# Kernel optimization log

Measured on AMD Instinct MI355X. Metric: run time of the kernel, lower is better.

Reference implementation:

```python
import jax, jax.numpy as jnp
import numpy as np

T = 512        # sentence length
V = 50000      # word vocab
NT = 50        # tag vocab
WD = 200       # word_dims
TD = 50        # tag_dims
U = 512        # lstm_units (per direction)
HID = 1024     # hidden_units
SOUT = 2       # struct_out
LOUT = 56      # label_out
NS = 8192      # number of struct span-sets
NL = 8192      # number of label span-sets
KS = 4         # struct_spans
KL = 3         # label_spans


def _spans(kl, kr, n, k):
    lefts = jax.random.randint(kl, (n, k), 1, T - 2)
    rights = jnp.minimum(lefts + jax.random.randint(kr, (n, k), 0, 16), T - 2)
    return lefts.astype(jnp.int32), rights.astype(jnp.int32)


def setup_inputs() -> dict:
    key = jax.random.key(0)
    ks = jax.random.split(key, 40)
    s = 0.02
    inp = {
        'word_inds': jax.random.randint(ks[0], (T,), 0, V).astype(jnp.int32),
        'tag_inds': jax.random.randint(ks[1], (T,), 0, NT).astype(jnp.int32),
        'struct_targets': jax.random.randint(ks[2], (NS,), 0, SOUT).astype(jnp.int32),
        'label_targets': jax.random.randint(ks[3], (NL,), 0, LOUT).astype(jnp.int32),
    }
    inp['struct_lefts'], inp['struct_rights'] = _spans(ks[4], ks[5], NS, KS)
    inp['label_lefts'], inp['label_rights'] = _spans(ks[6], ks[7], NL, KL)
    inp['W_word'] = jax.random.normal(ks[8], (V, WD), jnp.float32) * s
    inp['W_tag'] = jax.random.normal(ks[9], (NT, TD), jnp.float32) * s
    # LSTM params, PyTorch layout: W_ih [4U, in], W_hh [4U, U], bias [4U] (b_ih+b_hh fused)
    d0, d1 = WD + TD, 2 * U
    i = 10
    for name, din in [('l0f', d0), ('l0b', d0), ('l1f', d1), ('l1b', d1)]:
        inp['Wih_' + name] = jax.random.normal(ks[i], (4 * U, din), jnp.float32) * s; i += 1
        inp['Whh_' + name] = jax.random.normal(ks[i], (4 * U, U), jnp.float32) * s; i += 1
        inp['b_' + name] = jnp.zeros((4 * U,), jnp.float32)
    inp['Ws1'] = jax.random.normal(ks[i], (HID, 2 * KS * U), jnp.float32) * s; i += 1
    inp['bs1'] = jnp.zeros((HID,), jnp.float32)
    inp['Ws2'] = jax.random.normal(ks[i], (SOUT, HID), jnp.float32) * s; i += 1
    inp['bs2'] = jnp.zeros((SOUT,), jnp.float32)
    inp['Wl1'] = jax.random.normal(ks[i], (HID, 2 * KL * U), jnp.float32) * s; i += 1
    inp['bl1'] = jnp.zeros((HID,), jnp.float32)
    inp['Wl2'] = jax.random.normal(ks[i], (LOUT, HID), jnp.float32) * s; i += 1
    inp['bl2'] = jnp.zeros((LOUT,), jnp.float32)
    return inp


def _lstm_dir(x, Wih, Whh, b, reverse):
    # x: [T, Din] -> h sequence [T, U]; gate order i,f,g,o (PyTorch)
    xg = x @ Wih.T + b  # [T, 4U]
    u = Whh.shape[1]
    def step(carry, xt):
        h, c = carry
        g = xt + h @ Whh.T
        gi, gf, gg, go = jnp.split(g, 4)
        i = jax.nn.sigmoid(gi); f = jax.nn.sigmoid(gf)
        gg = jnp.tanh(gg); o = jax.nn.sigmoid(go)
        c = f * c + i * gg
        h = o * jnp.tanh(c)
        return (h, c), h
    init = (jnp.zeros((u,), x.dtype), jnp.zeros((u,), x.dtype))
    _, hs = jax.lax.scan(step, init, xg, reverse=reverse)
    return hs


def _span_loss(fwd, back, lefts, rights, targets, W1, b1, W2, b2):
    n = lefts.shape[0]
    f = fwd[rights] - fwd[lefts - 1]          # [N, K, U]
    bk = back[lefts] - back[rights + 1]       # [N, K, U]
    h = jnp.concatenate([f.reshape(n, -1), bk.reshape(n, -1)], axis=1)
    h = jax.nn.relu(h @ W1.T + b1)
    scores = h @ W2.T + b2
    logp = jax.nn.log_softmax(scores, axis=-1)
    return -jnp.take_along_axis(logp, targets[:, None], axis=1)[:, 0]


def reference(word_inds, tag_inds, struct_lefts, struct_rights, struct_targets,
              label_lefts, label_rights, label_targets,
              W_word, W_tag,
              Wih_l0f, Whh_l0f, b_l0f, Wih_l0b, Whh_l0b, b_l0b,
              Wih_l1f, Whh_l1f, b_l1f, Wih_l1b, Whh_l1b, b_l1b,
              Ws1, bs1, Ws2, bs2, Wl1, bl1, Wl2, bl2):
    x = jnp.concatenate([W_word[word_inds], W_tag[tag_inds]], axis=1)  # [T, WD+TD]
    h0 = jnp.concatenate([_lstm_dir(x, Wih_l0f, Whh_l0f, b_l0f, False),
                          _lstm_dir(x, Wih_l0b, Whh_l0b, b_l0b, True)], axis=1)
    out = jnp.concatenate([_lstm_dir(h0, Wih_l1f, Whh_l1f, b_l1f, False),
                           _lstm_dir(h0, Wih_l1b, Whh_l1b, b_l1b, True)], axis=1)  # [T, 2U]
    fwd, back = out[:, :U], out[:, U:]
    sl = _span_loss(fwd, back, struct_lefts, struct_rights, struct_targets, Ws1, bs1, Ws2, bs2)
    ll = _span_loss(fwd, back, label_lefts, label_rights, label_targets, Wl1, bl1, Wl2, bl2)
    return jnp.concatenate([sl, ll]).mean()
```

## Files before the change

kernel.cpp:

```cpp
#include <hip/hip_runtime.h>

using u16 = unsigned short;
using u32 = unsigned int;
using u64 = unsigned long long;
typedef __attribute__((ext_vector_type(8))) short bf16x8;
typedef __attribute__((ext_vector_type(4))) float f32x4;

__device__ __forceinline__ u16 f2b(float f) {
  u32 u = __float_as_uint(f);
  return (u16)((u + 0x7fffu + ((u >> 16) & 1u)) >> 16);
}

static constexpr size_t HEX_SZ    = (size_t)513 * 512 * 4;
static constexpr size_t OFF_HEXF0 = 0;
static constexpr size_t OFF_HEXB0 = OFF_HEXF0 + HEX_SZ;
static constexpr size_t OFF_HEXF1 = OFF_HEXB0 + HEX_SZ;
static constexpr size_t OFF_HEXB1 = OFF_HEXF1 + HEX_SZ;
static constexpr size_t OFF_LACC  = OFF_HEXB1 + HEX_SZ;
static constexpr size_t OFF_CLAIM = OFF_LACC + 1024;
static constexpr size_t OFF_PROG  = OFF_CLAIM + 256;
static constexpr size_t ZERO_BYTES= OFF_PROG + 4 * 262144;
static constexpr size_t OFF_XB    = ZERO_BYTES;
static constexpr size_t OFF_WIH0F = OFF_XB    + (size_t)512*256*2;
static constexpr size_t OFF_WIH0B = OFF_WIH0F + (size_t)2048*256*2;
static constexpr size_t OFF_WIH1F = OFF_WIH0B + (size_t)2048*256*2;
static constexpr size_t OFF_WIH1B = OFF_WIH1F + (size_t)2048*1024*2;
static constexpr size_t OFF_BSALL = OFF_WIH1B + (size_t)2048*1024*2;
static constexpr size_t OFF_BLALL = OFF_BSALL + (size_t)8192*512*2;
static constexpr size_t OFF_HCAT0 = OFF_BLALL + (size_t)6144*512*2;
static constexpr size_t OFF_HCAT1 = OFF_HCAT0 + (size_t)512*1024*2;
static constexpr size_t OFF_XG0F  = OFF_HCAT1 + (size_t)512*1024*2;
static constexpr size_t OFF_XG0B  = OFF_XG0F  + (size_t)512*2048*4;
static constexpr size_t OFF_XG1F  = OFF_XG0B  + (size_t)512*2048*4;
static constexpr size_t OFF_XG1B  = OFF_XG1F  + (size_t)512*2048*4;
static constexpr size_t OFF_PFS   = OFF_XG1B  + (size_t)512*2048*4;
static constexpr size_t OFF_PBS   = OFF_PFS   + (size_t)512*4096*4;
static constexpr size_t OFF_PFL   = OFF_PBS   + (size_t)512*4096*4;
static constexpr size_t OFF_PBL   = OFF_PFL   + (size_t)512*3072*4;

__global__ __launch_bounds__(64) void k_embed(const int* __restrict__ wi, const int* __restrict__ ti,
                                              const float* __restrict__ Ww, const float* __restrict__ Wt,
                                              u16* __restrict__ x) {
  int t = blockIdx.x;
  int w = wi[t], tg = ti[t];
  for (int c = threadIdx.x; c < 256; c += 64) {
    float v = 0.f;
    if (c < 200) v = Ww[(size_t)w * 200 + c];
    else if (c < 250) v = Wt[(size_t)tg * 50 + (c - 200)];
    x[(size_t)t * 256 + c] = f2b(v);
  }
}

__global__ __launch_bounds__(256) void k_prep_all(const float* __restrict__ Wih_l0f, const float* __restrict__ Wih_l0b,
                                                  u16* __restrict__ wih0f, u16* __restrict__ wih0b,
                                                  const float* __restrict__ Wih_l1f, const float* __restrict__ Wih_l1b,
                                                  u16* __restrict__ wih1f, u16* __restrict__ wih1b,
                                                  const float* __restrict__ Ws1, u16* __restrict__ bsall,
                                                  const float* __restrict__ Wl1, u16* __restrict__ blall) {
  int i0 = blockIdx.x * 256 + threadIdx.x, stride = gridDim.x * 256;
  for (int i = i0; i < 2048 * 256; i += stride) {
    int n = i >> 8, k = i & 255;
    wih0f[i] = (k < 250) ? f2b(Wih_l0f[(size_t)n * 250 + k]) : (u16)0;
    wih0b[i] = (k < 250) ? f2b(Wih_l0b[(size_t)n * 250 + k]) : (u16)0;
  }
  for (int i = i0; i < 2048 * 1024; i += stride) {
    wih1f[i] = f2b(Wih_l1f[i]);
    wih1b[i] = f2b(Wih_l1b[i]);
  }
  for (int i = i0; i < 8 * 1024 * 512; i += stride) {
    int u = i & 511, nidx = i >> 9, k = nidx >> 10, h = nidx & 1023;
    bsall[i] = f2b(Ws1[(size_t)h * 4096 + k * 512 + u]);
  }
  for (int i = i0; i < 6 * 1024 * 512; i += stride) {
    int u = i & 511, nidx = i >> 9, k = nidx >> 10, h = nidx & 1023;
    blall[i] = f2b(Wl1[(size_t)h * 3072 + k * 512 + u]);
  }
}

#define AST 40
__device__ __forceinline__ void gemm_body(const u16* __restrict__ A, int lda,
                                          const u16* __restrict__ B, int ldb,
                                          float* __restrict__ C, int ldc,
                                          const float* __restrict__ bias, int K,
                                          int m0, int n0) {
  __shared__ u16 As[128 * AST];
  __shared__ u16 Bs[128 * AST];
  int tid = threadIdx.x;
  int lane = tid & 63, wave = tid >> 6;
  int wm = wave >> 1, wn = wave & 1;
  f32x4 z = {0.f, 0.f, 0.f, 0.f};
  f32x4 acc[4][4];
#pragma unroll
  for (int i = 0; i < 4; ++i)
#pragma unroll
    for (int j = 0; j < 4; ++j) acc[i][j] = z;

  for (int k0 = 0; k0 < K; k0 += 32) {
#pragma unroll
    for (int it = 0; it < 2; ++it) {
      int c = tid + it * 256;
      int row = c >> 2, cc = (c & 3) << 3;
      *(bf16x8*)&As[row * AST + cc] = *(const bf16x8*)&A[(size_t)(m0 + row) * lda + k0 + cc];
      *(bf16x8*)&Bs[row * AST + cc] = *(const bf16x8*)&B[(size_t)(n0 + row) * ldb + k0 + cc];
    }
    __syncthreads();
    int rA = lane & 15, kk = (lane >> 4) << 3;
    bf16x8 af[4], bg[4];
#pragma unroll
    for (int i = 0; i < 4; ++i) {
      af[i] = *(const bf16x8*)&As[(wm * 64 + i * 16 + rA) * AST + kk];
      bg[i] = *(const bf16x8*)&Bs[(wn * 64 + i * 16 + rA) * AST + kk];
    }
#pragma unroll
    for (int i = 0; i < 4; ++i)
#pragma unroll
      for (int j = 0; j < 4; ++j)
        acc[i][j] = __builtin_amdgcn_mfma_f32_16x16x32_bf16(af[i], bg[j], acc[i][j], 0, 0, 0);
    __syncthreads();
  }
  int rg = (lane >> 4) << 2;
#pragma unroll
  for (int i = 0; i < 4; ++i)
#pragma unroll
    for (int j = 0; j < 4; ++j) {
      int n = n0 + wn * 64 + j * 16 + (lane & 15);
      float bv = bias ? bias[n] : 0.f;
#pragma unroll
      for (int r = 0; r < 4; ++r) {
        int m = m0 + wm * 64 + i * 16 + rg + r;
        C[(size_t)m * ldc + n] = acc[i][j][r] + bv;
      }
    }
}

__global__ __launch_bounds__(256) void k_gemm2(const u16* A, int lda,
                                               const u16* B0, const u16* B1, int ldb,
                                               float* C0, float* C1, int ldc,
                                               const float* bias0, const float* bias1, int K) {
  int z = blockIdx.z;
  gemm_body(A, lda, z ? B1 : B0, ldb, z ? C1 : C0, ldc, z ? bias1 : bias0, K,
            blockIdx.y * 128, blockIdx.x * 128);
}

__global__ __launch_bounds__(256) void k_proj(const u16* hcat1, const u16* bsall, const u16* blall,
                                              float* Pfs, float* Pbs, float* Pfl, float* Pbl) {
  int z = blockIdx.z;
  if (z >= 2 && blockIdx.x >= 24) return;
  const u16* A = (z & 1) ? (hcat1 + 512) : hcat1;
  const u16* B; float* C; int N;
  if (z == 0)      { B = bsall;                        C = Pfs; N = 4096; }
  else if (z == 1) { B = bsall + (size_t)4096 * 512;   C = Pbs; N = 4096; }
  else if (z == 2) { B = blall;                        C = Pfl; N = 3072; }
  else             { B = blall + (size_t)3072 * 512;   C = Pbl; N = 3072; }
  gemm_body(A, 1024, B, 512, C, N, nullptr, 512, blockIdx.y * 128, blockIdx.x * 128);
}

template <bool FAST>
__device__ __forceinline__ void lstm_core(int dir, int slice,
                                          const float* __restrict__ xg, const float* __restrict__ whh,
                                          u32* __restrict__ hex, u32* __restrict__ prog,
                                          u16* __restrict__ hcat) {
  __shared__ __align__(16) u16 hw[4][2][512];
  int tid = threadIdx.x;
  int wave = tid >> 6, lane = tid & 63;
  int col = lane & 15, kgrp = lane >> 4;
  int u0 = slice * 32;
  int uw = u0 + 8 * wave;

  bf16x8 bfr[2][16];
#pragma unroll
  for (int ntl = 0; ntl < 2; ++ntl) {
    int gate = 2 * ntl + (col >> 3);
    int row = gate * 512 + uw + (col & 7);
    const float* wr = whh + (size_t)row * 512;
#pragma unroll
    for (int kt = 0; kt < 16; ++kt) {
      int k0 = kt * 32 + kgrp * 8;
      f32x4 w0 = *(const f32x4*)&wr[k0];
      f32x4 w1 = *(const f32x4*)&wr[k0 + 4];
      bf16x8 v;
      v[0] = (short)f2b(w0.x); v[1] = (short)f2b(w0.y);
      v[2] = (short)f2b(w0.z); v[3] = (short)f2b(w0.w);
      v[4] = (short)f2b(w1.x); v[5] = (short)f2b(w1.y);
      v[6] = (short)f2b(w1.z); v[7] = (short)f2b(w1.w);
      bfr[ntl][kt] = v;
    }
  }

  const u64 TAGM = 0x0000FFFF0000FFFFull;
  float creg = 0.f;
  u32 it = (u32)(slice * 4 + wave);
  for (int s = 0; s < 512; ++s) {
    int t = dir ? (511 - s) : s;
    int rrow = dir ? (t + 1) : t;
    int par = s & 1;

    const float* xr = &xg[(size_t)t * 2048 + uw + (lane & 7)];
    float xga = xr[0], xgb2 = xr[512], xgc = xr[1024], xgd = xr[1536];

    u64 w0, w1, w2, w3;
    if constexpr (FAST) {
      for (;;) {
        u32 idx = (it++) & 63u;
        u32 p;
        if (idx == 0u)
          p = __hip_atomic_load(&prog[lane & 15], __ATOMIC_RELAXED, __HIP_MEMORY_SCOPE_AGENT);
        else
          p = __hip_atomic_load(&prog[(size_t)idx * 1024 + (lane & 15)], __ATOMIC_RELAXED, __HIP_MEMORY_SCOPE_WORKGROUP);
        if (__all((int)(p >= (u32)s))) break;
      }
      asm volatile("" ::: "memory");
      const u64* hp = (const u64*)(hex + (size_t)rrow * 512) + lane * 4;
      w0 = __hip_atomic_load(hp + 0, __ATOMIC_RELAXED, __HIP_MEMORY_SCOPE_WORKGROUP);
      w1 = __hip_atomic_load(hp + 1, __ATOMIC_RELAXED, __HIP_MEMORY_SCOPE_WORKGROUP);
      w2 = __hip_atomic_load(hp + 2, __ATOMIC_RELAXED, __HIP_MEMORY_SCOPE_WORKGROUP);
      w3 = __hip_atomic_load(hp + 3, __ATOMIC_RELAXED, __HIP_MEMORY_SCOPE_WORKGROUP);
    } else {
      const u64* hp = (const u64*)(hex + (size_t)rrow * 512) + lane * 4;
      u64 expct = (u64)(u32)s | ((u64)(u32)s << 32);
      do {
        w0 = __hip_atomic_load(hp + 0, __ATOMIC_RELAXED, __HIP_MEMORY_SCOPE_AGENT);
        w1 = __hip_atomic_load(hp + 1, __ATOMIC_RELAXED, __HIP_MEMORY_SCOPE_AGENT);
        w2 = __hip_atomic_load(hp + 2, __ATOMIC_RELAXED, __HIP_MEMORY_SCOPE_AGENT);
        w3 = __hip_atomic_load(hp + 3, __ATOMIC_RELAXED, __HIP_MEMORY_SCOPE_AGENT);
      } while (((w0 & TAGM) != expct) | ((w1 & TAGM) != expct) |
               ((w2 & TAGM) != expct) | ((w3 & TAGM) != expct));
    }

    bf16x8 hv;
    hv[0] = (short)(u16)(w0 >> 16); hv[1] = (short)(u16)(w0 >> 48);
    hv[2] = (short)(u16)(w1 >> 16); hv[3] = (short)(u16)(w1 >> 48);
    hv[4] = (short)(u16)(w2 >> 16); hv[5] = (short)(u16)(w2 >> 48);
    hv[6] = (short)(u16)(w3 >> 16); hv[7] = (short)(u16)(w3 >> 48);
    *(bf16x8*)&hw[wave][par][lane * 8] = hv;

    const u16* hb = &hw[wave][par][0];
    f32x4 z4 = {0.f, 0.f, 0.f, 0.f};
    f32x4 acc0[4], acc1[4];
#pragma unroll
    for (int q = 0; q < 4; ++q) { acc0[q] = z4; acc1[q] = z4; }
#pragma unroll
    for (int kt = 0; kt < 16; ++kt) {
      bf16x8 a = *(const bf16x8*)&hb[kt * 32 + kgrp * 8];
      acc0[kt & 3] = __builtin_amdgcn_mfma_f32_16x16x32_bf16(a, bfr[0][kt], acc0[kt & 3], 0, 0, 0);
      acc1[kt & 3] = __builtin_amdgcn_mfma_f32_16x16x32_bf16(a, bfr[1][kt], acc1[kt & 3], 0, 0, 0);
    }
    float v0 = acc0[0].x + acc0[1].x + acc0[2].x + acc0[3].x;
    float v1 = acc1[0].x + acc1[1].x + acc1[2].x + acc1[3].x;
    float gfv = __shfl_xor(v0, 8);
    float gov = __shfl_xor(v1, 8);
    if (lane < 8) {
      float gi = v0 + xga, gf = gfv + xgb2, gg = v1 + xgc, go = gov + xgd;
      float iv = __builtin_amdgcn_rcpf(1.f + __expf(-gi));
      float fv = __builtin_amdgcn_rcpf(1.f + __expf(-gf));
      float gv = 1.f - 2.f * __builtin_amdgcn_rcpf(__expf(2.f * gg) + 1.f);
      float ov = __builtin_amdgcn_rcpf(1.f + __expf(-go));
      creg = fv * creg + iv * gv;
      float h = ov * (1.f - 2.f * __builtin_amdgcn_rcpf(__expf(2.f * creg) + 1.f));
      u16 hb16 = f2b(h);
      int wrow = dir ? t : (t + 1);
      u32 word = ((u32)hb16 << 16) | (u32)(s + 1);
      if constexpr (FAST)
        __hip_atomic_store(&hex[(size_t)wrow * 512 + uw + lane], word, __ATOMIC_RELAXED, __HIP_MEMORY_SCOPE_WORKGROUP);
      else
        __hip_atomic_store(&hex[(size_t)wrow * 512 + uw + lane], word, __ATOMIC_RELAXED, __HIP_MEMORY_SCOPE_AGENT);
      hcat[(size_t)t * 1024 + dir * 512 + uw + lane] = hb16;
    }
    if constexpr (FAST) {
      __syncthreads();
      if (wave == 0) {
        if (lane == 0)
          __hip_atomic_store(&prog[slice], (u32)(s + 1), __ATOMIC_RELAXED, __HIP_MEMORY_SCOPE_AGENT);
        else
          __hip_atomic_store(&prog[(size_t)lane * 1024 + slice], (u32)(s + 1), __ATOMIC_RELAXED, __HIP_MEMORY_SCOPE_WORKGROUP);
      }
    }
  }
}

__global__ __launch_bounds__(256, 1) void k_lstm(const float* __restrict__ xg_f, const float* __restrict__ xg_b,
                                                 const float* __restrict__ whh_f, const float* __restrict__ whh_b,
                                                 u32* __restrict__ hex_f, u32* __restrict__ hex_b,
                                                 u32* __restrict__ claim,
                                                 u32* __restrict__ prog_f, u32* __restrict__ prog_b,
                                                 u16* __restrict__ hcat) {
  __shared__ int sh[3];
  if (threadIdx.x == 0) {
    u32 xcd;
    asm volatile("s_getreg_b32 %0, hwreg(HW_REG_XCC_ID)" : "=s"(xcd));
    xcd &= 7u;
    u32 slot = __hip_atomic_fetch_add(&claim[xcd], 1u, __ATOMIC_RELAXED, __HIP_MEMORY_SCOPE_AGENT);
    u32 tot  = __hip_atomic_fetch_add(&claim[8], 1u, __ATOMIC_ACQ_REL, __HIP_MEMORY_SCOPE_AGENT);
    if (tot == (u32)gridDim.x - 1u) {
      u32 c0 = __hip_atomic_load(&claim[0], __ATOMIC_RELAXED, __HIP_MEMORY_SCOPE_AGENT);
      u32 c1 = __hip_atomic_load(&claim[1], __ATOMIC_RELAXED, __HIP_MEMORY_SCOPE_AGENT);
      __hip_atomic_store(&claim[9], (c0 >= 16u && c1 >= 16u) ? 1u : 2u,
                         __ATOMIC_RELEASE, __HIP_MEMORY_SCOPE_AGENT);
    }
    u32 m;
    do { m = __hip_atomic_load(&claim[9], __ATOMIC_ACQUIRE, __HIP_MEMORY_SCOPE_AGENT); } while (m == 0u);
    int dir = -1, slice = 0;
    if (m == 1u) {
      if (xcd == 0u && slot < 16u)      { dir = 0; slice = (int)slot; }
      else if (xcd == 1u && slot < 16u) { dir = 1; slice = (int)slot; }
    } else {
      u32 s2 = __hip_atomic_fetch_add(&claim[10], 1u, __ATOMIC_RELAXED, __HIP_MEMORY_SCOPE_AGENT);
      if (s2 < 32u) { dir = (int)(s2 >> 4); slice = (int)(s2 & 15u); }
    }
    sh[0] = dir; sh[1] = slice; sh[2] = (m == 1u) ? 1 : 0;
  }
  __syncthreads();
  int dir = sh[0], slice = sh[1], fast = sh[2];
  if (dir < 0) return;
  const float* xg  = dir ? xg_b : xg_f;
  const float* whh = dir ? whh_b : whh_f;
  u32* hex  = dir ? hex_b : hex_f;
  u32* prog = dir ? prog_b : prog_f;
  if (fast) lstm_core<true>(dir, slice, xg, whh, hex, prog, hcat);
  else      lstm_core<false>(dir, slice, xg, whh, hex, prog, hcat);
}

template <int KSP, int C>
__device__ __forceinline__ void span_body(int blk,
                                          const float* __restrict__ Pf, const float* __restrict__ Pb,
                                          const int* __restrict__ lefts, const int* __restrict__ rights,
                                          const int* __restrict__ tgts, const float* __restrict__ b1,
                                          const float* __restrict__ W2, const float* __restrict__ b2,
                                          float* __restrict__ loss_acc) {
  constexpr int NP = KSP * 1024;
  __shared__ float hid[4][1024];
  __shared__ float sc[4][64];
  int tid = threadIdx.x;
  int n0 = blk * 4;
  int d = tid * 4;
  f32x4 bv = *(const f32x4*)&b1[d];
#pragma unroll
  for (int ss = 0; ss < 4; ++ss) {
    int n = n0 + ss;
    f32x4 acc = bv;
#pragma unroll
    for (int k = 0; k < KSP; ++k) {
      int l = lefts[n * KSP + k], r = rights[n * KSP + k];
      f32x4 a1 = *(const f32x4*)&Pf[(size_t)r * NP + k * 1024 + d];
      f32x4 a2 = *(const f32x4*)&Pf[(size_t)(l - 1) * NP + k * 1024 + d];
      f32x4 a3 = *(const f32x4*)&Pb[(size_t)l * NP + k * 1024 + d];
      f32x4 a4 = *(const f32x4*)&Pb[(size_t)(r + 1) * NP + k * 1024 + d];
      acc += a1 - a2 + a3 - a4;
    }
    acc.x = fmaxf(acc.x, 0.f); acc.y = fmaxf(acc.y, 0.f);
    acc.z = fmaxf(acc.z, 0.f); acc.w = fmaxf(acc.w, 0.f);
    *(f32x4*)&hid[ss][d] = acc;
  }
  __syncthreads();
  int wave = tid >> 6, lane = tid & 63;
  for (int c = wave; c < C; c += 4) {
    float p0 = 0.f, p1 = 0.f, p2 = 0.f, p3 = 0.f;
    for (int i = lane; i < 1024; i += 64) {
      float w = W2[(size_t)c * 1024 + i];
      p0 += hid[0][i] * w; p1 += hid[1][i] * w; p2 += hid[2][i] * w; p3 += hid[3][i] * w;
    }
#pragma unroll
    for (int o = 32; o; o >>= 1) {
      p0 += __shfl_xor(p0, o); p1 += __shfl_xor(p1, o);
      p2 += __shfl_xor(p2, o); p3 += __shfl_xor(p3, o);
    }
    if (lane == 0) {
      sc[0][c] = p0 + b2[c]; sc[1][c] = p1 + b2[c];
      sc[2][c] = p2 + b2[c]; sc[3][c] = p3 + b2[c];
    }
  }
  __syncthreads();
  {
    int s = wave;
    float v = (lane < C) ? sc[s][lane] : -1e30f;
    float m = v;
#pragma unroll
    for (int o = 32; o; o >>= 1) m = fmaxf(m, __shfl_xor(m, o));
    float e = (lane < C) ? __expf(v - m) : 0.f;
#pragma unroll
    for (int o = 32; o; o >>= 1) e += __shfl_xor(e, o);
    if (lane == 0) {
      int tg = tgts[n0 + s];
      float loss = m + __logf(e) - sc[s][tg];
      atomicAdd(&loss_acc[(n0 + s) & 255], loss);
    }
  }
}

__global__ __launch_bounds__(256) void k_span_fused(const float* Pfs, const float* Pbs,
                                                    const int* s_l, const int* s_r, const int* s_tgt,
                                                    const float* bs1, const float* Ws2, const float* bs2,
                                                    const float* Pfl, const float* Pbl,
                                                    const int* l_l, const int* l_r, const int* l_tgt,
                                                    const float* bl1, const float* Wl2, const float* bl2,
                                                    float* lacc) {
  if (blockIdx.x < 2048)
    span_body<4, 2>(blockIdx.x, Pfs, Pbs, s_l, s_r, s_tgt, bs1, Ws2, bs2, lacc);
  else
    span_body<3, 56>(blockIdx.x - 2048, Pfl, Pbl, l_l, l_r, l_tgt, bl1, Wl2, bl2, lacc);
}

__global__ __launch_bounds__(256) void k_finalize(const float* __restrict__ acc, float* __restrict__ out) {
  int tid = threadIdx.x;
  __shared__ float s[4];
  float v = acc[tid];
#pragma unroll
  for (int o = 32; o; o >>= 1) v += __shfl_xor(v, o);
  if ((tid & 63) == 0) s[tid >> 6] = v;
  __syncthreads();
  if (tid == 0) out[0] = (s[0] + s[1] + s[2] + s[3]) * (1.0f / 16384.0f);
}

extern "C" void kernel_launch(void* const* d_in, const int* in_sizes, int n_in,
                              void* d_out, int out_size, void* d_ws, size_t ws_size,
                              hipStream_t stream) {
  (void)in_sizes; (void)n_in; (void)out_size; (void)ws_size;
  const int* word_inds = (const int*)d_in[0];
  const int* tag_inds  = (const int*)d_in[1];
  const int* s_tgt = (const int*)d_in[2];
  const int* l_tgt = (const int*)d_in[3];
  const int* s_l = (const int*)d_in[4];
  const int* s_r = (const int*)d_in[5];
  const int* l_l = (const int*)d_in[6];
  const int* l_r = (const int*)d_in[7];
  const float* W_word  = (const float*)d_in[8];
  const float* W_tag   = (const float*)d_in[9];
  const float* Wih_l0f = (const float*)d_in[10];
  const float* Whh_l0f = (const float*)d_in[11];
  const float* b_l0f   = (const float*)d_in[12];
  const float* Wih_l0b = (const float*)d_in[13];
  const float* Whh_l0b = (const float*)d_in[14];
  const float* b_l0b   = (const float*)d_in[15];
  const float* Wih_l1f = (const float*)d_in[16];
  const float* Whh_l1f = (const float*)d_in[17];
  const float* b_l1f   = (const float*)d_in[18];
  const float* Wih_l1b = (const float*)d_in[19];
  const float* Whh_l1b = (const float*)d_in[20];
  const float* b_l1b   = (const float*)d_in[21];
  const float* Ws1 = (const float*)d_in[22];
  const float* bs1 = (const float*)d_in[23];
  const float* Ws2 = (const float*)d_in[24];
  const float* bs2 = (const float*)d_in[25];
  const float* Wl1 = (const float*)d_in[26];
  const float* bl1 = (const float*)d_in[27];
  const float* Wl2 = (const float*)d_in[28];
  const float* bl2 = (const float*)d_in[29];

  char* ws = (char*)d_ws;
  u32* hexf0 = (u32*)(ws + OFF_HEXF0);
  u32* hexb0 = (u32*)(ws + OFF_HEXB0);
  u32* hexf1 = (u32*)(ws + OFF_HEXF1);
  u32* hexb1 = (u32*)(ws + OFF_HEXB1);
  float* lacc = (float*)(ws + OFF_LACC);
  u32* claim0 = (u32*)(ws + OFF_CLAIM);
  u32* claim1 = (u32*)(ws + OFF_CLAIM + 64);
  u32* progf0 = (u32*)(ws + OFF_PROG);
  u32* progb0 = (u32*)(ws + OFF_PROG + 262144);
  u32* progf1 = (u32*)(ws + OFF_PROG + 2 * 262144);
  u32* progb1 = (u32*)(ws + OFF_PROG + 3 * 262144);
  u16* xb    = (u16*)(ws + OFF_XB);
  u16* wih0f = (u16*)(ws + OFF_WIH0F);
  u16* wih0b = (u16*)(ws + OFF_WIH0B);
  u16* wih1f = (u16*)(ws + OFF_WIH1F);
  u16* wih1b = (u16*)(ws + OFF_WIH1B);
  u16* bsall = (u16*)(ws + OFF_BSALL);
  u16* blall = (u16*)(ws + OFF_BLALL);
  u16* hcat0 = (u16*)(ws + OFF_HCAT0);
  u16* hcat1 = (u16*)(ws + OFF_HCAT1);
  float* xg0f = (float*)(ws + OFF_XG0F);
  float* xg0b = (float*)(ws + OFF_XG0B);
  float* xg1f = (float*)(ws + OFF_XG1F);
  float* xg1b = (float*)(ws + OFF_XG1B);
  float* Pfs = (float*)(ws + OFF_PFS);
  float* Pbs = (float*)(ws + OFF_PBS);
  float* Pfl = (float*)(ws + OFF_PFL);
  float* Pbl = (float*)(ws + OFF_PBL);

  hipMemsetAsync(ws, 0, ZERO_BYTES, stream);

  k_embed<<<512, 64, 0, stream>>>(word_inds, tag_inds, W_word, W_tag, xb);
  k_prep_all<<<1024, 256, 0, stream>>>(Wih_l0f, Wih_l0b, wih0f, wih0b,
                                       Wih_l1f, Wih_l1b, wih1f, wih1b,
                                       Ws1, bsall, Wl1, blall);

  k_gemm2<<<dim3(16, 4, 2), 256, 0, stream>>>(xb, 256, wih0f, wih0b, 256, xg0f, xg0b, 2048, b_l0f, b_l0b, 256);
  k_lstm<<<256, 256, 0, stream>>>(xg0f, xg0b, Whh_l0f, Whh_l0b, hexf0, hexb0, claim0, progf0, progb0, hcat0);
  k_gemm2<<<dim3(16, 4, 2), 256, 0, stream>>>(hcat0, 1024, wih1f, wih1b, 1024, xg1f, xg1b, 2048, b_l1f, b_l1b, 1024);
  k_lstm<<<256, 256, 0, stream>>>(xg1f, xg1b, Whh_l1f, Whh_l1b, hexf1, hexb1, claim1, progf1, progb1, hcat1);

  k_proj<<<dim3(32, 4, 4), 256, 0, stream>>>(hcat1, bsall, blall, Pfs, Pbs, Pfl, Pbl);

  k_span_fused<<<4096, 256, 0, stream>>>(Pfs, Pbs, s_l, s_r, s_tgt, bs1, Ws2, bs2,
                                         Pfl, Pbl, l_l, l_r, l_tgt, bl1, Wl2, bl2, lacc);
  k_finalize<<<1, 256, 0, stream>>>(lacc, (float*)d_out);
}
```

Before: 2.008 ms.

## Replace LSTM progress-flag sync with tagged polling, bf16 projections, xg prefetch

The LSTM recurrence drops the per-step __syncthreads plus progress-counter broadcast. Each wave now polls the tagged h-exchange rows directly with sc0 loads, and every eighth retry falls back to an agent-scope shadow copy. Gate input terms are prefetched into LDS every 64 steps, the span projections are stored as bf16 to halve span-kernel traffic, and the large memset becomes a tiny zeroing kernel that clears only the boundary rows. The intent is to shorten the per-step serial latency of the recurrence, at the cost of extra duplicate stores, some visibility risk from the cache-level polling, and bf16 rounding on the projection outputs.

```diff
diff --git a/kernel.cpp b/kernel.cpp
--- a/kernel.cpp
+++ b/kernel.cpp
@@ -10,17 +10,20 @@
   u32 u = __float_as_uint(f);
   return (u16)((u + 0x7fffu + ((u >> 16) & 1u)) >> 16);
 }
+__device__ __forceinline__ float b2f(u16 v) { return __uint_as_float(((u32)v) << 16); }
 
 static constexpr size_t HEX_SZ    = (size_t)513 * 512 * 4;
 static constexpr size_t OFF_HEXF0 = 0;
 static constexpr size_t OFF_HEXB0 = OFF_HEXF0 + HEX_SZ;
 static constexpr size_t OFF_HEXF1 = OFF_HEXB0 + HEX_SZ;
 static constexpr size_t OFF_HEXB1 = OFF_HEXF1 + HEX_SZ;
-static constexpr size_t OFF_LACC  = OFF_HEXB1 + HEX_SZ;
+static constexpr size_t OFF_HSF0  = OFF_HEXB1 + HEX_SZ;
+static constexpr size_t OFF_HSB0  = OFF_HSF0  + HEX_SZ;
+static constexpr size_t OFF_HSF1  = OFF_HSB0  + HEX_SZ;
+static constexpr size_t OFF_HSB1  = OFF_HSF1  + HEX_SZ;
+static constexpr size_t OFF_LACC  = OFF_HSB1  + HEX_SZ;
 static constexpr size_t OFF_CLAIM = OFF_LACC + 1024;
-static constexpr size_t OFF_PROG  = OFF_CLAIM + 256;
-static constexpr size_t ZERO_BYTES= OFF_PROG + 4 * 262144;
-static constexpr size_t OFF_XB    = ZERO_BYTES;
+static constexpr size_t OFF_XB    = OFF_CLAIM + 256;
 static constexpr size_t OFF_WIH0F = OFF_XB    + (size_t)512*256*2;
 static constexpr size_t OFF_WIH0B = OFF_WIH0F + (size_t)2048*256*2;
 static constexpr size_t OFF_WIH1F = OFF_WIH0B + (size_t)2048*256*2;
@@ -34,9 +37,22 @@
 static constexpr size_t OFF_XG1F  = OFF_XG0B  + (size_t)512*2048*4;
 static constexpr size_t OFF_XG1B  = OFF_XG1F  + (size_t)512*2048*4;
 static constexpr size_t OFF_PFS   = OFF_XG1B  + (size_t)512*2048*4;
-static constexpr size_t OFF_PBS   = OFF_PFS   + (size_t)512*4096*4;
-static constexpr size_t OFF_PFL   = OFF_PBS   + (size_t)512*4096*4;
-static constexpr size_t OFF_PBL   = OFF_PFL   + (size_t)512*3072*4;
+static constexpr size_t OFF_PBS   = OFF_PFS   + (size_t)512*4096*2;
+static constexpr size_t OFF_PFL   = OFF_PBS   + (size_t)512*4096*2;
+static constexpr size_t OFF_PBL   = OFF_PFL   + (size_t)512*3072*2;
+
+__global__ __launch_bounds__(256) void k_zero(u32* hf0, u32* hb0, u32* hf1, u32* hb1,
+                                              u32* sf0, u32* sb0, u32* sf1, u32* sb1,
+                                              u32* lacc, u32* claims) {
+  int tid = threadIdx.x;
+  for (int i = tid; i < 512; i += 256) {
+    size_t o = (size_t)512 * 512 + i;
+    hf0[i] = 0; hf1[i] = 0; sf0[i] = 0; sf1[i] = 0;
+    hb0[o] = 0; hb1[o] = 0; sb0[o] = 0; sb1[o] = 0;
+  }
+  lacc[tid] = 0;
+  if (tid < 64) claims[tid] = 0;
+}
 
 __global__ __launch_bounds__(64) void k_embed(const int* __restrict__ wi, const int* __restrict__ ti,
                                               const float* __restrict__ Ww, const float* __restrict__ Wt,
@@ -78,9 +94,10 @@
 }
 
 #define AST 40
+template <bool BF16OUT>
 __device__ __forceinline__ void gemm_body(const u16* __restrict__ A, int lda,
                                           const u16* __restrict__ B, int ldb,
-                                          float* __restrict__ C, int ldc,
+                                          void* __restrict__ Cv, int ldc,
                                           const float* __restrict__ bias, int K,
                                           int m0, int n0) {
   __shared__ u16 As[128 * AST];
@@ -128,7 +145,8 @@
 #pragma unroll
       for (int r = 0; r < 4; ++r) {
         int m = m0 + wm * 64 + i * 16 + rg + r;
-        C[(size_t)m * ldc + n] = acc[i][j][r] + bv;
+        if constexpr (BF16OUT) ((u16*)Cv)[(size_t)m * ldc + n] = f2b(acc[i][j][r] + bv);
+        else                   ((float*)Cv)[(size_t)m * ldc + n] = acc[i][j][r] + bv;
       }
     }
 }
@@ -138,29 +156,30 @@
                                                float* C0, float* C1, int ldc,
                                                const float* bias0, const float* bias1, int K) {
   int z = blockIdx.z;
-  gemm_body(A, lda, z ? B1 : B0, ldb, z ? C1 : C0, ldc, z ? bias1 : bias0, K,
-            blockIdx.y * 128, blockIdx.x * 128);
+  gemm_body<false>(A, lda, z ? B1 : B0, ldb, z ? C1 : C0, ldc, z ? bias1 : bias0, K,
+                   blockIdx.y * 128, blockIdx.x * 128);
 }
 
 __global__ __launch_bounds__(256) void k_proj(const u16* hcat1, const u16* bsall, const u16* blall,
-                                              float* Pfs, float* Pbs, float* Pfl, float* Pbl) {
+                                              u16* Pfs, u16* Pbs, u16* Pfl, u16* Pbl) {
   int z = blockIdx.z;
   if (z >= 2 && blockIdx.x >= 24) return;
   const u16* A = (z & 1) ? (hcat1 + 512) : hcat1;
-  const u16* B; float* C; int N;
+  const u16* B; u16* C; int N;
   if (z == 0)      { B = bsall;                        C = Pfs; N = 4096; }
   else if (z == 1) { B = bsall + (size_t)4096 * 512;   C = Pbs; N = 4096; }
   else if (z == 2) { B = blall;                        C = Pfl; N = 3072; }
   else             { B = blall + (size_t)3072 * 512;   C = Pbl; N = 3072; }
-  gemm_body(A, 1024, B, 512, C, N, nullptr, 512, blockIdx.y * 128, blockIdx.x * 128);
+  gemm_body<true>(A, 1024, B, 512, C, N, nullptr, 512, blockIdx.y * 128, blockIdx.x * 128);
 }
 
 template <bool FAST>
 __device__ __forceinline__ void lstm_core(int dir, int slice,
                                           const float* __restrict__ xg, const float* __restrict__ whh,
-                                          u32* __restrict__ hex, u32* __restrict__ prog,
+                                          u32* __restrict__ hex, u32* __restrict__ hexS,
                                           u16* __restrict__ hcat) {
   __shared__ __align__(16) u16 hw[4][2][512];
+  __shared__ __align__(16) float xgl[4][64][32];
   int tid = threadIdx.x;
   int wave = tid >> 6, lane = tid & 63;
   int col = lane & 15, kgrp = lane >> 4;
@@ -189,42 +208,49 @@
 
   const u64 TAGM = 0x0000FFFF0000FFFFull;
   float creg = 0.f;
-  u32 it = (u32)(slice * 4 + wave);
   for (int s = 0; s < 512; ++s) {
+    if ((s & 63) == 0) {
+      int e = lane;
+      int te = dir ? (511 - (s + e)) : (s + e);
+      const float* xr = &xg[(size_t)te * 2048 + uw];
+      float* dst = &xgl[wave][e][0];
+#pragma unroll
+      for (int g = 0; g < 4; ++g) {
+        *(f32x4*)&dst[g * 8]     = *(const f32x4*)&xr[g * 512];
+        *(f32x4*)&dst[g * 8 + 4] = *(const f32x4*)&xr[g * 512 + 4];
+      }
+    }
     int t = dir ? (511 - s) : s;
     int rrow = dir ? (t + 1) : t;
     int par = s & 1;
 
-    const float* xr = &xg[(size_t)t * 2048 + uw + (lane & 7)];
-    float xga = xr[0], xgb2 = xr[512], xgc = xr[1024], xgd = xr[1536];
-
+    const u64* hp  = (const u64*)(hex  + (size_t)rrow * 512) + lane * 4;
+    const u64* hpS = (const u64*)(hexS + (size_t)rrow * 512) + lane * 4;
+    u64 expct = (u64)(u32)s | ((u64)(u32)s << 32);
     u64 w0, w1, w2, w3;
-    if constexpr (FAST) {
-      for (;;) {
-        u32 idx = (it++) & 63u;
-        u32 p;
-        if (idx == 0u)
-          p = __hip_atomic_load(&prog[lane & 15], __ATOMIC_RELAXED, __HIP_MEMORY_SCOPE_AGENT);
-        else
-          p = __hip_atomic_load(&prog[(size_t)idx * 1024 + (lane & 15)], __ATOMIC_RELAXED, __HIP_MEMORY_SCOPE_WORKGROUP);
-        if (__all((int)(p >= (u32)s))) break;
+    u32 rnd = 0;
+    for (;;) {
+      bool fastld = FAST && ((rnd++ & 7u) != 7u);
+      if (fastld) {
+        asm volatile(
+            "global_load_dwordx2 %0, %4, off sc0\n\t"
+            "global_load_dwordx2 %1, %4, off offset:8 sc0\n\t"
+            "global_load_dwordx2 %2, %4, off offset:16 sc0\n\t"
+            "global_load_dwordx2 %3, %4, off offset:24 sc0\n\t"
+            "s_waitcnt vmcnt(0)"
+            : "=&v"(w0), "=&v"(w1), "=&v"(w2), "=&v"(w3)
+            : "v"(hp)
+            : "memory");
+      } else {
+        const u64* p = FAST ? hpS : hp;
+        w0 = __hip_atomic_load(p + 0, __ATOMIC_RELAXED, __HIP_MEMORY_SCOPE_AGENT);
+        w1 = __hip_atomic_load(p + 1, __ATOMIC_RELAXED, __HIP_MEMORY_SCOPE_AGENT);
+        w2 = __hip_atomic_load(p + 2, __ATOMIC_RELAXED, __HIP_MEMORY_SCOPE_AGENT);
+        w3 = __hip_atomic_load(p + 3, __ATOMIC_RELAXED, __HIP_MEMORY_SCOPE_AGENT);
       }
-      asm volatile("" ::: "memory");
-      const u64* hp = (const u64*)(hex + (size_t)rrow * 512) + lane * 4;
-      w0 = __hip_atomic_load(hp + 0, __ATOMIC_RELAXED, __HIP_MEMORY_SCOPE_WORKGROUP);
-      w1 = __hip_atomic_load(hp + 1, __ATOMIC_RELAXED, __HIP_MEMORY_SCOPE_WORKGROUP);
-      w2 = __hip_atomic_load(hp + 2, __ATOMIC_RELAXED, __HIP_MEMORY_SCOPE_WORKGROUP);
-      w3 = __hip_atomic_load(hp + 3, __ATOMIC_RELAXED, __HIP_MEMORY_SCOPE_WORKGROUP);
-    } else {
-      const u64* hp = (const u64*)(hex + (size_t)rrow * 512) + lane * 4;
-      u64 expct = (u64)(u32)s | ((u64)(u32)s << 32);
-      do {
-        w0 = __hip_atomic_load(hp + 0, __ATOMIC_RELAXED, __HIP_MEMORY_SCOPE_AGENT);
-        w1 = __hip_atomic_load(hp + 1, __ATOMIC_RELAXED, __HIP_MEMORY_SCOPE_AGENT);
-        w2 = __hip_atomic_load(hp + 2, __ATOMIC_RELAXED, __HIP_MEMORY_SCOPE_AGENT);
-        w3 = __hip_atomic_load(hp + 3, __ATOMIC_RELAXED, __HIP_MEMORY_SCOPE_AGENT);
-      } while (((w0 & TAGM) != expct) | ((w1 & TAGM) != expct) |
-               ((w2 & TAGM) != expct) | ((w3 & TAGM) != expct));
+      if (!(((w0 & TAGM) != expct) | ((w1 & TAGM) != expct) |
+            ((w2 & TAGM) != expct) | ((w3 & TAGM) != expct)))
+        break;
     }
 
     bf16x8 hv;
@@ -250,6 +276,8 @@
     float gfv = __shfl_xor(v0, 8);
     float gov = __shfl_xor(v1, 8);
     if (lane < 8) {
+      const float* xe = &xgl[wave][s & 63][0];
+      float xga = xe[lane], xgb2 = xe[8 + lane], xgc = xe[16 + lane], xgd = xe[24 + lane];
       float gi = v0 + xga, gf = gfv + xgb2, gg = v1 + xgc, go = gov + xgd;
       float iv = __builtin_amdgcn_rcpf(1.f + __expf(-gi));
       float fv = __builtin_amdgcn_rcpf(1.f + __expf(-gf));
@@ -260,20 +288,14 @@
       u16 hb16 = f2b(h);
       int wrow = dir ? t : (t + 1);
       u32 word = ((u32)hb16 << 16) | (u32)(s + 1);
-      if constexpr (FAST)
-        __hip_atomic_store(&hex[(size_t)wrow * 512 + uw + lane], word, __ATOMIC_RELAXED, __HIP_MEMORY_SCOPE_WORKGROUP);
-      else
-        __hip_atomic_store(&hex[(size_t)wrow * 512 + uw + lane], word, __ATOMIC_RELAXED, __HIP_MEMORY_SCOPE_AGENT);
+      size_t idx = (size_t)wrow * 512 + uw + lane;
+      if constexpr (FAST) {
+        __hip_atomic_store(&hex[idx], word, __ATOMIC_RELAXED, __HIP_MEMORY_SCOPE_WORKGROUP);
+        __hip_atomic_store(&hexS[idx], word, __ATOMIC_RELAXED, __HIP_MEMORY_SCOPE_AGENT);
+      } else {
+        __hip_atomic_store(&hex[idx], word, __ATOMIC_RELAXED, __HIP_MEMORY_SCOPE_AGENT);
+      }
       hcat[(size_t)t * 1024 + dir * 512 + uw + lane] = hb16;
-    }
-    if constexpr (FAST) {
-      __syncthreads();
-      if (wave == 0) {
-        if (lane == 0)
-          __hip_atomic_store(&prog[slice], (u32)(s + 1), __ATOMIC_RELAXED, __HIP_MEMORY_SCOPE_AGENT);
-        else
-          __hip_atomic_store(&prog[(size_t)lane * 1024 + slice], (u32)(s + 1), __ATOMIC_RELAXED, __HIP_MEMORY_SCOPE_WORKGROUP);
-      }
     }
   }
 }
@@ -281,8 +303,8 @@
 __global__ __launch_bounds__(256, 1) void k_lstm(const float* __restrict__ xg_f, const float* __restrict__ xg_b,
                                                  const float* __restrict__ whh_f, const float* __restrict__ whh_b,
                                                  u32* __restrict__ hex_f, u32* __restrict__ hex_b,
+                                                 u32* __restrict__ hs_f, u32* __restrict__ hs_b,
                                                  u32* __restrict__ claim,
-                                                 u32* __restrict__ prog_f, u32* __restrict__ prog_b,
                                                  u16* __restrict__ hcat) {
   __shared__ int sh[3];
   if (threadIdx.x == 0) {
@@ -314,15 +336,15 @@
   if (dir < 0) return;
   const float* xg  = dir ? xg_b : xg_f;
   const float* whh = dir ? whh_b : whh_f;
-  u32* hex  = dir ? hex_b : hex_f;
-  u32* prog = dir ? prog_b : prog_f;
-  if (fast) lstm_core<true>(dir, slice, xg, whh, hex, prog, hcat);
-  else      lstm_core<false>(dir, slice, xg, whh, hex, prog, hcat);
+  u32* hex = dir ? hex_b : hex_f;
+  u32* hs  = dir ? hs_b : hs_f;
+  if (fast) lstm_core<true>(dir, slice, xg, whh, hex, hs, hcat);
+  else      lstm_core<false>(dir, slice, xg, whh, hex, hs, hcat);
 }
 
 template <int KSP, int C>
 __device__ __forceinline__ void span_body(int blk,
-                                          const float* __restrict__ Pf, const float* __restrict__ Pb,
+                                          const u16* __restrict__ Pf, const u16* __restrict__ Pb,
                                           const int* __restrict__ lefts, const int* __restrict__ rights,
                                           const int* __restrict__ tgts, const float* __restrict__ b1,
                                           const float* __restrict__ W2, const float* __restrict__ b2,
@@ -341,11 +363,14 @@
 #pragma unroll
     for (int k = 0; k < KSP; ++k) {
       int l = lefts[n * KSP + k], r = rights[n * KSP + k];
-      f32x4 a1 = *(const f32x4*)&Pf[(size_t)r * NP + k * 1024 + d];
-      f32x4 a2 = *(const f32x4*)&Pf[(size_t)(l - 1) * NP + k * 1024 + d];
-      f32x4 a3 = *(const f32x4*)&Pb[(size_t)l * NP + k * 1024 + d];
-      f32x4 a4 = *(const f32x4*)&Pb[(size_t)(r + 1) * NP + k * 1024 + d];
-      acc += a1 - a2 + a3 - a4;
+      ushort4 a1 = *(const ushort4*)&Pf[(size_t)r * NP + k * 1024 + d];
+      ushort4 a2 = *(const ushort4*)&Pf[(size_t)(l - 1) * NP + k * 1024 + d];
+      ushort4 a3 = *(const ushort4*)&Pb[(size_t)l * NP + k * 1024 + d];
+      ushort4 a4 = *(const ushort4*)&Pb[(size_t)(r + 1) * NP + k * 1024 + d];
+      acc.x += b2f(a1.x) - b2f(a2.x) + b2f(a3.x) - b2f(a4.x);
+      acc.y += b2f(a1.y) - b2f(a2.y) + b2f(a3.y) - b2f(a4.y);
+      acc.z += b2f(a1.z) - b2f(a2.z) + b2f(a3.z) - b2f(a4.z);
+      acc.w += b2f(a1.w) - b2f(a2.w) + b2f(a3.w) - b2f(a4.w);
     }
     acc.x = fmaxf(acc.x, 0.f); acc.y = fmaxf(acc.y, 0.f);
     acc.z = fmaxf(acc.z, 0.f); acc.w = fmaxf(acc.w, 0.f);
@@ -387,10 +412,10 @@
   }
 }
 
-__global__ __launch_bounds__(256) void k_span_fused(const float* Pfs, const float* Pbs,
+__global__ __launch_bounds__(256) void k_span_fused(const u16* Pfs, const u16* Pbs,
                                                     const int* s_l, const int* s_r, const int* s_tgt,
                                                     const float* bs1, const float* Ws2, const float* bs2,
-                                                    const float* Pfl, const float* Pbl,
+                                                    const u16* Pfl, const u16* Pbl,
                                                     const int* l_l, const int* l_r, const int* l_tgt,
                                                     const float* bl1, const float* Wl2, const float* bl2,
                                                     float* lacc) {
@@ -451,13 +476,13 @@
   u32* hexb0 = (u32*)(ws + OFF_HEXB0);
   u32* hexf1 = (u32*)(ws + OFF_HEXF1);
   u32* hexb1 = (u32*)(ws + OFF_HEXB1);
+  u32* hsf0  = (u32*)(ws + OFF_HSF0);
+  u32* hsb0  = (u32*)(ws + OFF_HSB0);
+  u32* hsf1  = (u32*)(ws + OFF_HSF1);
+  u32* hsb1  = (u32*)(ws + OFF_HSB1);
   float* lacc = (float*)(ws + OFF_LACC);
   u32* claim0 = (u32*)(ws + OFF_CLAIM);
   u32* claim1 = (u32*)(ws + OFF_CLAIM + 64);
-  u32* progf0 = (u32*)(ws + OFF_PROG);
-  u32* progb0 = (u32*)(ws + OFF_PROG + 262144);
-  u32* progf1 = (u32*)(ws + OFF_PROG + 2 * 262144);
-  u32* progb1 = (u32*)(ws + OFF_PROG + 3 * 262144);
   u16* xb    = (u16*)(ws + OFF_XB);
   u16* wih0f = (u16*)(ws + OFF_WIH0F);
   u16* wih0b = (u16*)(ws + OFF_WIH0B);
@@ -471,22 +496,22 @@
   float* xg0b = (float*)(ws + OFF_XG0B);
   float* xg1f = (float*)(ws + OFF_XG1F);
   float* xg1b = (float*)(ws + OFF_XG1B);
-  float* Pfs = (float*)(ws + OFF_PFS);
-  float* Pbs = (float*)(ws + OFF_PBS);
-  float* Pfl = (float*)(ws + OFF_PFL);
-  float* Pbl = (float*)(ws + OFF_PBL);
-
-  hipMemsetAsync(ws, 0, ZERO_BYTES, stream);
-
+  u16* Pfs = (u16*)(ws + OFF_PFS);
+  u16* Pbs = (u16*)(ws + OFF_PBS);
+  u16* Pfl = (u16*)(ws + OFF_PFL);
+  u16* Pbl = (u16*)(ws + OFF_PBL);
+
+  k_zero<<<1, 256, 0, stream>>>(hexf0, hexb0, hexf1, hexb1, hsf0, hsb0, hsf1, hsb1,
+                                (u32*)lacc, claim0);
   k_embed<<<512, 64, 0, stream>>>(word_inds, tag_inds, W_word, W_tag, xb);
   k_prep_all<<<1024, 256, 0, stream>>>(Wih_l0f, Wih_l0b, wih0f, wih0b,
                                        Wih_l1f, Wih_l1b, wih1f, wih1b,
                                        Ws1, bsall, Wl1, blall);
 
   k_gemm2<<<dim3(16, 4, 2), 256, 0, stream>>>(xb, 256, wih0f, wih0b, 256, xg0f, xg0b, 2048, b_l0f, b_l0b, 256);
-  k_lstm<<<256, 256, 0, stream>>>(xg0f, xg0b, Whh_l0f, Whh_l0b, hexf0, hexb0, claim0, progf0, progb0, hcat0);
+  k_lstm<<<256, 256, 0, stream>>>(xg0f, xg0b, Whh_l0f, Whh_l0b, hexf0, hexb0, hsf0, hsb0, claim0, hcat0);
   k_gemm2<<<dim3(16, 4, 2), 256, 0, stream>>>(hcat0, 1024, wih1f, wih1b, 1024, xg1f, xg1b, 2048, b_l1f, b_l1b, 1024);
-  k_lstm<<<256, 256, 0, stream>>>(xg1f, xg1b, Whh_l1f, Whh_l1b, hexf1, hexb1, claim1, progf1, progb1, hcat1);
+  k_lstm<<<256, 256, 0, stream>>>(xg1f, xg1b, Whh_l1f, Whh_l1b, hexf1, hexb1, hsf1, hsb1, claim1, hcat1);
 
   k_proj<<<dim3(32, 4, 4), 256, 0, stream>>>(hcat1, bsall, blall, Pfs, Pbs, Pfl, Pbl);
 
```

Result: slower. 2.595 ms (+29.2%).
